# Kernel optimization log

Hardware: AMD Instinct MI355X
Metric: run time of the kernel (lower is better)

The kernel has to match this reference:

```python
import jax, jax.numpy as jnp
import numpy as np

NUM_EMBED = 512
EMBED_DIM = 64
COMMITMENT_COST = 0.25
DECAY = 0.99
LAPLACE_ALPHA = 1e-05


def setup_inputs() -> dict:
    key = jax.random.key(0)
    k1, k2 = jax.random.split(key, 2)
    inputs = jax.random.normal(k1, (4, EMBED_DIM, 32, 32, 32), dtype=jnp.float32)
    embed = jax.random.normal(k2, (NUM_EMBED, EMBED_DIM), dtype=jnp.float32)
    # buffers: embed_avg starts as a clone of embed; cluster_size at steady state (post first pass)
    embed_avg = embed
    cluster_size = jnp.ones((NUM_EMBED,), dtype=jnp.float32)
    return {"inputs": inputs, "embed": embed, "embed_avg": embed_avg, "cluster_size": cluster_size}


def reference(inputs, embed, embed_avg, cluster_size):
    # channel-last flatten: [B,C,D,H,W] -> [B,D,H,W,C] -> [N,C]
    channel_last = jnp.transpose(inputs, (0, 2, 3, 4, 1))
    input_shape = channel_last.shape
    flat_input = channel_last.reshape(-1, EMBED_DIM)  # [N, C]
    n_tokens = flat_input.shape[0]

    distances = ((flat_input ** 2).sum(axis=1, keepdims=True)
                 + (embed ** 2).sum(axis=1)
                 - 2.0 * flat_input @ embed.T)
    encoding_indices = jnp.argmin(distances, axis=1)  # [N]

    quantized_cl = embed[encoding_indices].reshape(input_shape)  # gather + reshape

    # --- EMA codebook update (training branch), all non-differentiable ---
    # new_cluster_size = one_hot.sum(0); dw = one_hot.T @ flat_input  (as segment sums)
    new_counts = jax.ops.segment_sum(jnp.ones((n_tokens,), flat_input.dtype),
                                     encoding_indices, num_segments=NUM_EMBED)
    dw = jax.ops.segment_sum(flat_input, encoding_indices, num_segments=NUM_EMBED)  # [K, C]
    new_cluster_size = cluster_size * DECAY + (1.0 - DECAY) * new_counts
    new_embed_avg = embed_avg * DECAY + (1.0 - DECAY) * dw
    n = new_cluster_size.sum()
    smoothed = n * ((new_cluster_size + LAPLACE_ALPHA) / (n + NUM_EMBED * LAPLACE_ALPHA))
    new_embed = new_embed_avg / smoothed[:, None]

    # perplexity from empirical code usage
    avg_probs = new_counts / n_tokens
    perplexity = jnp.exp(-jnp.sum(avg_probs * jnp.log(avg_probs + 1e-10)))

    quantized_cf = jnp.transpose(quantized_cl, (0, 4, 1, 2, 3))  # back to [B,C,D,H,W]

    # commitment loss (quantized is detached in original; everything above is no_grad)
    e_latent_loss = jnp.mean((quantized_cf - inputs) ** 2)
    loss = COMMITMENT_COST * e_latent_loss

    # straight-through estimator
    quantized_out = inputs + jax.lax.stop_gradient(quantized_cf - inputs)

    encoding_indices = encoding_indices.reshape(input_shape[:-1])
    return (loss, quantized_out, perplexity, encoding_indices,
            new_embed, new_cluster_size, new_embed_avg)
```

## Files before the change

kernel.cpp:

```cpp
#include <hip/hip_runtime.h>
#include <math.h>

typedef __attribute__((ext_vector_type(8))) short s16x8;
typedef __attribute__((ext_vector_type(4))) float f32x4;

#define B_    4
#define C_    64
#define S_    32768
#define N_    131072
#define K_    512
#define SPLITS 8
#define DECAY_ 0.99f
#define ONEM_  0.01f
#define ALPHA_ 1e-5f
#define DELTA_ 0.01f
#define AMB_CAP 65536

#define OFF_LOSS 0
#define OFF_Q    1
#define OFF_PERP 8388609
#define OFF_IDX  8388610
#define OFF_NEMB 8519682
#define OFF_NCS  8552450
#define OFF_NEA  8552962

#define WS_LOSS   0
#define WS_AMBN   8
#define WS_CNT    16
#define WS_CUR    528
#define WS_OFFS   1040
#define WS_SMOOTH 1552
#define WS_E2     2064
#define WS_SORT   2576
#define WS_PART   133648
#define WS_SPL    395792
#define WS_AMB    444944
#define WS_ET     510480

__device__ __forceinline__ ushort f2bf(float f) {
    uint u = __float_as_uint(f);
    u = u + 0x7FFFu + ((u >> 16) & 1u);
    return (ushort)(u >> 16);
}
__device__ __forceinline__ float bf2f(ushort h) {
    return __uint_as_float(((uint)h) << 16);
}

__global__ __launch_bounds__(256) void k_split(const float* __restrict__ embed,
                                               float* __restrict__ wsf,
                                               int* __restrict__ wsi) {
    const int t = threadIdx.x;
    const int lane = t & 63;
    const int code = blockIdx.x * 4 + (t >> 6);
    if (blockIdx.x == 0) {
        for (int i = t; i < WS_OFFS; i += 256) wsi[i] = 0;
    }
    const float e = embed[code * C_ + lane];
    const float sc = -2.f * e;
    const ushort h1 = f2bf(sc);
    const ushort h2 = f2bf(sc - bf2f(h1));
    ushort* tab = (ushort*)(wsf + WS_SPL);
    tab[0 * (K_ * C_) + code * C_ + lane] = h1;
    tab[1 * (K_ * C_) + code * C_ + lane] = h2;
    wsf[WS_ET + lane * K_ + code] = e;
    float sq = e * e;
    for (int o = 32; o > 0; o >>= 1) sq += __shfl_down(sq, o, 64);
    if (lane == 0) wsf[WS_E2 + code] = sq;
}

__global__ __launch_bounds__(256) void k_assign(const float* __restrict__ in,
                                                float* __restrict__ out,
                                                float* __restrict__ wsf,
                                                int* __restrict__ wsi) {
    __shared__ float s_e2l[K_];
    __shared__ int   s_cnt[K_];
    __shared__ float s_x2[256];
    __shared__ float s_loss;

    const int t = threadIdx.x;
    const int lane = t & 63;
    const int w = t >> 6;
    const int col = lane & 15;
    const int quad = lane >> 4;

    for (int i = t; i < K_; i += 256) { s_e2l[i] = wsf[WS_E2 + i]; s_cnt[i] = 0; }
    if (t == 0) s_loss = 0.f;

    const int nw = blockIdx.x * 256 + w * 64;

    s16x8 a[4][2][2];
#pragma unroll
    for (int j = 0; j < 4; ++j) {
        const int n = nw + j * 16 + col;
        const int base = ((n >> 15) << 21) + (n & (S_ - 1));
        float x0[8], x1[8];
#pragma unroll
        for (int q = 0; q < 8; ++q) {
            x0[q] = in[base + ((quad * 8 + q) << 15)];
            x1[q] = in[base + ((32 + quad * 8 + q) << 15)];
        }
        float x2 = 0.f;
#pragma unroll
        for (int q = 0; q < 8; ++q) x2 += x0[q] * x0[q] + x1[q] * x1[q];
        x2 += __shfl_xor(x2, 16, 64);
        x2 += __shfl_xor(x2, 32, 64);
        if (quad == 0) s_x2[w * 64 + j * 16 + col] = x2;

        float4* q0 = (float4*)(out + OFF_Q + (size_t)n * C_ + quad * 8);
        q0[0] = make_float4(x0[0], x0[1], x0[2], x0[3]);
        q0[1] = make_float4(x0[4], x0[5], x0[6], x0[7]);
        float4* q1 = (float4*)(out + OFF_Q + (size_t)n * C_ + 32 + quad * 8);
        q1[0] = make_float4(x1[0], x1[1], x1[2], x1[3]);
        q1[1] = make_float4(x1[4], x1[5], x1[6], x1[7]);

#pragma unroll
        for (int q = 0; q < 8; ++q) {
            ushort h = f2bf(x0[q]); a[j][0][0][q] = (short)h;
            a[j][1][0][q] = (short)f2bf(x0[q] - bf2f(h));
            h = f2bf(x1[q]); a[j][0][1][q] = (short)h;
            a[j][1][1][q] = (short)f2bf(x1[q] - bf2f(h));
        }
    }
    __syncthreads();

    const s16x8* tab = (const s16x8*)(wsf + WS_SPL);
    float bestd[4][4], bestd2[4][4];
    int   besti[4][4];
#pragma unroll
    for (int j = 0; j < 4; ++j)
#pragma unroll
        for (int r = 0; r < 4; ++r) { bestd[j][r] = 3.4e38f; bestd2[j][r] = 3.4e38f; besti[j][r] = 0; }

    int o = col * 8 + quad;
    s16x8 bh0 = tab[o], bh1 = tab[o + 4];
    s16x8 bl0 = tab[4096 + o], bl1 = tab[4096 + o + 4];

    for (int ct = 0; ct < 32; ++ct) {
        s16x8 nh0, nh1, nl0, nl1;
        if (ct < 31) {
            const int on = o + 128;
            nh0 = tab[on];        nh1 = tab[on + 4];
            nl0 = tab[4096 + on]; nl1 = tab[4096 + on + 4];
        }
        const float e2c = s_e2l[ct * 16 + col];
        f32x4 acc[4];
#pragma unroll
        for (int j = 0; j < 4; ++j) acc[j] = (f32x4){e2c, e2c, e2c, e2c};
#pragma unroll
        for (int j = 0; j < 4; ++j) acc[j] = __builtin_amdgcn_mfma_f32_16x16x32_bf16(a[j][1][0], bh0, acc[j], 0, 0, 0);
#pragma unroll
        for (int j = 0; j < 4; ++j) acc[j] = __builtin_amdgcn_mfma_f32_16x16x32_bf16(a[j][1][1], bh1, acc[j], 0, 0, 0);
#pragma unroll
        for (int j = 0; j < 4; ++j) acc[j] = __builtin_amdgcn_mfma_f32_16x16x32_bf16(a[j][0][0], bl0, acc[j], 0, 0, 0);
#pragma unroll
        for (int j = 0; j < 4; ++j) acc[j] = __builtin_amdgcn_mfma_f32_16x16x32_bf16(a[j][0][1], bl1, acc[j], 0, 0, 0);
#pragma unroll
        for (int j = 0; j < 4; ++j) acc[j] = __builtin_amdgcn_mfma_f32_16x16x32_bf16(a[j][0][0], bh0, acc[j], 0, 0, 0);
#pragma unroll
        for (int j = 0; j < 4; ++j) acc[j] = __builtin_amdgcn_mfma_f32_16x16x32_bf16(a[j][0][1], bh1, acc[j], 0, 0, 0);

        const int code = ct * 16 + col;
#pragma unroll
        for (int j = 0; j < 4; ++j) {
#pragma unroll
            for (int r = 0; r < 4; ++r) {
                const float av = acc[j][r];
                bestd2[j][r] = fminf(bestd2[j][r], fmaxf(av, bestd[j][r]));
                if (av < bestd[j][r]) { bestd[j][r] = av; besti[j][r] = code; }
            }
        }
        bh0 = nh0; bh1 = nh1; bl0 = nl0; bl1 = nl1;
        o += 128;
    }

    float lsum = 0.f;
#pragma unroll
    for (int j = 0; j < 4; ++j) {
#pragma unroll
        for (int r = 0; r < 4; ++r) {
            float d1 = bestd[j][r], d2 = bestd2[j][r]; int i1 = besti[j][r];
            for (int m = 1; m <= 8; m <<= 1) {
                const float d1o = __shfl_xor(d1, m, 64);
                const int   i1o = __shfl_xor(i1, m, 64);
                const float d2o = __shfl_xor(d2, m, 64);
                if (d1o < d1 || (d1o == d1 && i1o < i1)) {
                    d2 = fminf(d1, d2o); d1 = d1o; i1 = i1o;
                } else {
                    d2 = fminf(d2, d1o);
                }
            }
            if (col == 0) {
                const int tok = j * 16 + quad * 4 + r;
                out[OFF_IDX + nw + tok] = (float)i1;
                atomicAdd(&s_cnt[i1], 1);
                lsum += d1 + s_x2[w * 64 + tok];
                if (d2 - d1 < DELTA_) {
                    const int pos = atomicAdd(&wsi[WS_AMBN], 1);
                    if (pos < AMB_CAP) wsi[WS_AMB + pos] = nw + tok;
                }
            }
        }
    }
    if (col == 0) atomicAdd(&s_loss, lsum);
    __syncthreads();
    for (int i = t; i < K_; i += 256) {
        const int v = s_cnt[i];
        if (v) atomicAdd(&wsi[WS_CNT + i], v);
    }
    if (t == 0) atomicAdd(&wsf[WS_LOSS], s_loss);
}

__global__ __launch_bounds__(256) void k_fixup(float* __restrict__ out,
                                               const float* __restrict__ wsf,
                                               int* __restrict__ wsi) {
    __shared__ float sx[4][C_];
    const int t = threadIdx.x;
    const int lane = t & 63;
    const int w = t >> 6;
    const int gw = blockIdx.x * 4 + w;
    const int nw = gridDim.x * 4;
    int cntA = wsi[WS_AMBN];
    if (cntA > AMB_CAP) cntA = AMB_CAP;
    const float* eT = wsf + WS_ET;

    for (int a = gw; a < cntA; a += nw) {
        const int n = wsi[WS_AMB + a];
        const float xv = out[OFF_Q + (size_t)n * C_ + lane];
        sx[w][lane] = xv;
        float x2 = xv * xv;
        for (int m = 1; m <= 32; m <<= 1) x2 += __shfl_xor(x2, m, 64);

        float bd = 3.4e38f; int bi = 0;
#pragma unroll 2
        for (int q = 0; q < 8; ++q) {
            const int k = (q << 6) + lane;
            float d0 = 0.f, d1 = 0.f, d2 = 0.f, d3 = 0.f;
#pragma unroll
            for (int c = 0; c < C_; c += 4) {
                d0 += sx[w][c + 0] * eT[(c + 0) * K_ + k];
                d1 += sx[w][c + 1] * eT[(c + 1) * K_ + k];
                d2 += sx[w][c + 2] * eT[(c + 2) * K_ + k];
                d3 += sx[w][c + 3] * eT[(c + 3) * K_ + k];
            }
            const float dist = x2 + wsf[WS_E2 + k] - 2.f * ((d0 + d1) + (d2 + d3));
            if (dist < bd) { bd = dist; bi = k; }
        }
        for (int m = 1; m <= 32; m <<= 1) {
            const float db = __shfl_xor(bd, m, 64);
            const int   ib = __shfl_xor(bi, m, 64);
            if (db < bd || (db == bd && ib < bi)) { bd = db; bi = ib; }
        }
        if (lane == 0) {
            const int old = (int)out[OFF_IDX + n];
            if (bi != old) {
                out[OFF_IDX + n] = (float)bi;
                atomicAdd(&wsi[WS_CNT + old], -1);
                atomicAdd(&wsi[WS_CNT + bi], 1);
            }
        }
    }
}

#define SCT 1024
__global__ __launch_bounds__(256) void k_scatter(const float* __restrict__ out,
                                                 int* __restrict__ wsi) {
    __shared__ int sA[K_];
    __shared__ int sB[K_];
    __shared__ int lc[K_];
    __shared__ int codes[SCT];
    const int t = threadIdx.x;
    const int base = blockIdx.x * SCT;

    const int c0 = wsi[WS_CNT + t];
    const int c1 = wsi[WS_CNT + t + 256];
    sA[t] = c0; sA[t + 256] = c1;
    __syncthreads();
    int* sa = sA; int* sb = sB;
    for (int o = 1; o < K_; o <<= 1) {
        const int va = sa[t]       + ((t >= o)       ? sa[t - o]       : 0);
        const int vb = sa[t + 256] + ((t + 256 >= o) ? sa[t + 256 - o] : 0);
        sb[t] = va; sb[t + 256] = vb;
        __syncthreads();
        int* tmp = sa; sa = sb; sb = tmp;
    }
    const int offs0 = sa[t] - c0;
    const int offs1 = sa[t + 256] - c1;
    if (blockIdx.x == 0) { wsi[WS_OFFS + t] = offs0; wsi[WS_OFFS + t + 256] = offs1; }

    int* hist = sb;
    hist[t] = 0; hist[t + 256] = 0;
    lc[t] = 0;  lc[t + 256] = 0;
    __syncthreads();
#pragma unroll
    for (int j = 0; j < SCT / 256; ++j) {
        const int k = (int)out[OFF_IDX + base + j * 256 + t];
        codes[j * 256 + t] = k;
        atomicAdd(&hist[k], 1);
    }
    __syncthreads();
    const int ha = hist[t];
    const int hb = hist[t + 256];
    int ga = 0, gb = 0;
    if (ha > 0) ga = atomicAdd(&wsi[WS_CUR + t], ha);
    if (hb > 0) gb = atomicAdd(&wsi[WS_CUR + t + 256], hb);
    __syncthreads();
    hist[t] = offs0 + ga;
    hist[t + 256] = offs1 + gb;
    __syncthreads();
#pragma unroll
    for (int j = 0; j < SCT / 256; ++j) {
        const int k = codes[j * 256 + t];
        const int pos = atomicAdd(&lc[k], 1);
        wsi[WS_SORT + hist[k] + pos] = base + j * 256 + t;
    }
}

__global__ __launch_bounds__(64) void k_dw_split(float* __restrict__ out,
                                                 float* __restrict__ wsf,
                                                 const int* __restrict__ wsi) {
    const int lane = threadIdx.x;
    const int k = blockIdx.x >> 3;
    const int p = blockIdx.x & (SPLITS - 1);
    const int off = wsi[WS_OFFS + k];
    const int cnt = wsi[WS_CNT + k];
    const int chunk = (cnt + SPLITS - 1) >> 3;
    const int j0 = p * chunk;
    const int j1 = min(j0 + chunk, cnt);
    const float* fx = out + OFF_Q;
    const int* sort = wsi + WS_SORT + off;

    float acc = 0.f;
    for (int base = j0; base < j1; base += 64) {
        const int mcnt = min(64, j1 - base);
        int id = 0;
        if (base + lane < j1) id = sort[base + lane];
        int m = 0;
        for (; m + 8 <= mcnt; m += 8) {
            const int t0 = __shfl(id, m + 0, 64);
            const int t1 = __shfl(id, m + 1, 64);
            const int t2 = __shfl(id, m + 2, 64);
            const int t3 = __shfl(id, m + 3, 64);
            const int t4 = __shfl(id, m + 4, 64);
            const int t5 = __shfl(id, m + 5, 64);
            const int t6 = __shfl(id, m + 6, 64);
            const int t7 = __shfl(id, m + 7, 64);
            const float v0 = fx[(size_t)t0 * C_ + lane];
            const float v1 = fx[(size_t)t1 * C_ + lane];
            const float v2 = fx[(size_t)t2 * C_ + lane];
            const float v3 = fx[(size_t)t3 * C_ + lane];
            const float v4 = fx[(size_t)t4 * C_ + lane];
            const float v5 = fx[(size_t)t5 * C_ + lane];
            const float v6 = fx[(size_t)t6 * C_ + lane];
            const float v7 = fx[(size_t)t7 * C_ + lane];
            acc += ((v0 + v1) + (v2 + v3)) + ((v4 + v5) + (v6 + v7));
        }
        for (; m < mcnt; ++m) {
            const int tk = __shfl(id, m, 64);
            acc += fx[(size_t)tk * C_ + lane];
        }
    }
    wsf[WS_PART + (size_t)blockIdx.x * C_ + lane] = acc;
}

__global__ __launch_bounds__(256) void k_emaq(const float* __restrict__ embed,
                                              const float* __restrict__ embed_avg,
                                              const float* __restrict__ cs,
                                              float* __restrict__ out,
                                              const float* __restrict__ wsf,
                                              const int* __restrict__ wsi) {
    __shared__ float sn[256];
    __shared__ float sncs[K_];
    const int t = threadIdx.x;
    const int bid = blockIdx.x;

    const int c0 = wsi[WS_CNT + t];
    const int c1 = wsi[WS_CNT + t + 256];
    const float ncs0 = cs[t] * DECAY_ + ONEM_ * (float)c0;
    const float ncs1 = cs[t + 256] * DECAY_ + ONEM_ * (float)c1;
    sncs[t] = ncs0; sncs[t + 256] = ncs1;
    sn[t] = ncs0 + ncs1;
    __syncthreads();
    for (int o = 128; o > 0; o >>= 1) { if (t < o) sn[t] += sn[t + o]; __syncthreads(); }
    const float ntot = sn[0];
    __syncthreads();

    if (bid == 0) {
        out[OFF_NCS + t] = ncs0;
        out[OFF_NCS + t + 256] = ncs1;
        const float ap0 = (float)c0 / (float)N_;
        const float ap1 = (float)c1 / (float)N_;
        sn[t] = ap0 * logf(ap0 + 1e-10f) + ap1 * logf(ap1 + 1e-10f);
        __syncthreads();
        for (int o = 128; o > 0; o >>= 1) { if (t < o) sn[t] += sn[t + o]; __syncthreads(); }
        if (t == 0) {
            out[OFF_PERP] = expf(-sn[0]);
            out[OFF_LOSS] = 0.25f * wsf[WS_LOSS] / (float)((long long)N_ * C_);
        }
    }

    if (bid < 128) {
        const int i = bid * 256 + t;
        const int k = i >> 6;
        const int c = i & 63;
        const float smooth = ntot * (sncs[k] + ALPHA_) / (ntot + (float)K_ * ALPHA_);
        float dw = 0.f;
#pragma unroll
        for (int p = 0; p < SPLITS; ++p)
            dw += wsf[WS_PART + (size_t)(k * SPLITS + p) * C_ + c];
        const float nea = embed_avg[i] * DECAY_ + ONEM_ * dw;
        out[OFF_NEA + i] = nea;
        out[OFF_NEMB + i] = nea / smooth;
    }

    const int n = bid * 256 + t;
    const int b = n >> 15;
    const int s = n & (S_ - 1);
    const int qbase = (b << 21) + s;
    const int k = (int)out[OFF_IDX + n];
    const float4* er = (const float4*)(embed + k * C_);
#pragma unroll
    for (int q = 0; q < 16; ++q) {
        float4 v = er[q];
        out[OFF_Q + qbase + ((4 * q + 0) << 15)] = v.x;
        out[OFF_Q + qbase + ((4 * q + 1) << 15)] = v.y;
        out[OFF_Q + qbase + ((4 * q + 2) << 15)] = v.z;
        out[OFF_Q + qbase + ((4 * q + 3) << 15)] = v.w;
    }
}

extern "C" void kernel_launch(void* const* d_in, const int* in_sizes, int n_in,
                              void* d_out, int out_size, void* d_ws, size_t ws_size,
                              hipStream_t stream) {
    const float* in        = (const float*)d_in[0];
    const float* embed     = (const float*)d_in[1];
    const float* embed_avg = (const float*)d_in[2];
    const float* cs        = (const float*)d_in[3];
    float* out = (float*)d_out;
    float* wsf = (float*)d_ws;
    int*   wsi = (int*)d_ws;

    k_split   <<<K_ / 4, 256, 0, stream>>>(embed, wsf, wsi);
    k_assign  <<<N_ / 256, 256, 0, stream>>>(in, out, wsf, wsi);
    k_fixup   <<<256, 256, 0, stream>>>(out, wsf, wsi);
    k_scatter <<<N_ / SCT, 256, 0, stream>>>(out, wsi);
    k_dw_split<<<K_ * SPLITS, 64, 0, stream>>>(out, wsf, wsi);
    k_emaq    <<<N_ / 256, 256, 0, stream>>>(embed, embed_avg, cs, out, wsf, wsi);
}
```

Baseline: 203.5 us.

## Fuse five post-split kernels into one persistent kernel with grid barriers

Merges the assign, fixup, scatter, dw-split and EMA/quantize kernels into a single 512-block kernel. The stages are separated by software grid-wide barriers built on an atomic counter in workspace. This removes four kernel launches and their inter-kernel gaps. The risks are spin-wait cost at each barrier, fewer blocks for the fixup and dw phases, and deadlock if the 512 blocks cannot all be resident at once.

```diff
diff --git a/kernel.cpp b/kernel.cpp
--- a/kernel.cpp
+++ b/kernel.cpp
@@ -15,6 +15,7 @@
 #define ALPHA_ 1e-5f
 #define DELTA_ 0.01f
 #define AMB_CAP 65536
+#define NB_   512
 
 #define OFF_LOSS 0
 #define OFF_Q    1
@@ -29,7 +30,7 @@
 #define WS_CNT    16
 #define WS_CUR    528
 #define WS_OFFS   1040
-#define WS_SMOOTH 1552
+#define WS_BAR    1552
 #define WS_E2     2064
 #define WS_SORT   2576
 #define WS_PART   133648
@@ -44,6 +45,17 @@
 }
 __device__ __forceinline__ float bf2f(ushort h) {
     return __uint_as_float(((uint)h) << 16);
+}
+
+__device__ __forceinline__ void gbar(int* bar, int target) {
+    __syncthreads();
+    if (threadIdx.x == 0) {
+        __threadfence();
+        atomicAdd(bar, 1);
+        while (atomicAdd(bar, 0) < target) __builtin_amdgcn_s_sleep(8);
+        __threadfence();
+    }
+    __syncthreads();
 }
 
 __global__ __launch_bounds__(256) void k_split(const float* __restrict__ embed,
@@ -54,6 +66,7 @@
     const int code = blockIdx.x * 4 + (t >> 6);
     if (blockIdx.x == 0) {
         for (int i = t; i < WS_OFFS; i += 256) wsi[i] = 0;
+        if (t == 0) wsi[WS_BAR] = 0;
     }
     const float e = embed[code * C_ + lane];
     const float sc = -2.f * e;
@@ -68,363 +81,361 @@
     if (lane == 0) wsf[WS_E2 + code] = sq;
 }
 
-__global__ __launch_bounds__(256) void k_assign(const float* __restrict__ in,
-                                                float* __restrict__ out,
-                                                float* __restrict__ wsf,
-                                                int* __restrict__ wsi) {
-    __shared__ float s_e2l[K_];
-    __shared__ int   s_cnt[K_];
-    __shared__ float s_x2[256];
-    __shared__ float s_loss;
+#define SCT 1024
+__global__ __launch_bounds__(256) void k_fused(const float* __restrict__ in,
+                                               const float* __restrict__ embed,
+                                               const float* __restrict__ embed_avg,
+                                               const float* __restrict__ cs,
+                                               float* __restrict__ out,
+                                               float* wsf,
+                                               int* wsi) {
+    __shared__ int smem[2560];
+    int* bar = wsi + WS_BAR;
 
     const int t = threadIdx.x;
+    const int bid = blockIdx.x;
     const int lane = t & 63;
     const int w = t >> 6;
-    const int col = lane & 15;
-    const int quad = lane >> 4;
-
-    for (int i = t; i < K_; i += 256) { s_e2l[i] = wsf[WS_E2 + i]; s_cnt[i] = 0; }
-    if (t == 0) s_loss = 0.f;
-
-    const int nw = blockIdx.x * 256 + w * 64;
-
-    s16x8 a[4][2][2];
-#pragma unroll
-    for (int j = 0; j < 4; ++j) {
-        const int n = nw + j * 16 + col;
-        const int base = ((n >> 15) << 21) + (n & (S_ - 1));
-        float x0[8], x1[8];
-#pragma unroll
-        for (int q = 0; q < 8; ++q) {
-            x0[q] = in[base + ((quad * 8 + q) << 15)];
-            x1[q] = in[base + ((32 + quad * 8 + q) << 15)];
-        }
-        float x2 = 0.f;
-#pragma unroll
-        for (int q = 0; q < 8; ++q) x2 += x0[q] * x0[q] + x1[q] * x1[q];
-        x2 += __shfl_xor(x2, 16, 64);
-        x2 += __shfl_xor(x2, 32, 64);
-        if (quad == 0) s_x2[w * 64 + j * 16 + col] = x2;
-
-        float4* q0 = (float4*)(out + OFF_Q + (size_t)n * C_ + quad * 8);
-        q0[0] = make_float4(x0[0], x0[1], x0[2], x0[3]);
-        q0[1] = make_float4(x0[4], x0[5], x0[6], x0[7]);
-        float4* q1 = (float4*)(out + OFF_Q + (size_t)n * C_ + 32 + quad * 8);
-        q1[0] = make_float4(x1[0], x1[1], x1[2], x1[3]);
-        q1[1] = make_float4(x1[4], x1[5], x1[6], x1[7]);
-
-#pragma unroll
-        for (int q = 0; q < 8; ++q) {
-            ushort h = f2bf(x0[q]); a[j][0][0][q] = (short)h;
-            a[j][1][0][q] = (short)f2bf(x0[q] - bf2f(h));
-            h = f2bf(x1[q]); a[j][0][1][q] = (short)h;
-            a[j][1][1][q] = (short)f2bf(x1[q] - bf2f(h));
-        }
-    }
-    __syncthreads();
-
-    const s16x8* tab = (const s16x8*)(wsf + WS_SPL);
-    float bestd[4][4], bestd2[4][4];
-    int   besti[4][4];
-#pragma unroll
-    for (int j = 0; j < 4; ++j)
-#pragma unroll
-        for (int r = 0; r < 4; ++r) { bestd[j][r] = 3.4e38f; bestd2[j][r] = 3.4e38f; besti[j][r] = 0; }
-
-    int o = col * 8 + quad;
-    s16x8 bh0 = tab[o], bh1 = tab[o + 4];
-    s16x8 bl0 = tab[4096 + o], bl1 = tab[4096 + o + 4];
-
-    for (int ct = 0; ct < 32; ++ct) {
-        s16x8 nh0, nh1, nl0, nl1;
-        if (ct < 31) {
-            const int on = o + 128;
-            nh0 = tab[on];        nh1 = tab[on + 4];
-            nl0 = tab[4096 + on]; nl1 = tab[4096 + on + 4];
-        }
-        const float e2c = s_e2l[ct * 16 + col];
-        f32x4 acc[4];
-#pragma unroll
-        for (int j = 0; j < 4; ++j) acc[j] = (f32x4){e2c, e2c, e2c, e2c};
-#pragma unroll
-        for (int j = 0; j < 4; ++j) acc[j] = __builtin_amdgcn_mfma_f32_16x16x32_bf16(a[j][1][0], bh0, acc[j], 0, 0, 0);
-#pragma unroll
-        for (int j = 0; j < 4; ++j) acc[j] = __builtin_amdgcn_mfma_f32_16x16x32_bf16(a[j][1][1], bh1, acc[j], 0, 0, 0);
-#pragma unroll
-        for (int j = 0; j < 4; ++j) acc[j] = __builtin_amdgcn_mfma_f32_16x16x32_bf16(a[j][0][0], bl0, acc[j], 0, 0, 0);
-#pragma unroll
-        for (int j = 0; j < 4; ++j) acc[j] = __builtin_amdgcn_mfma_f32_16x16x32_bf16(a[j][0][1], bl1, acc[j], 0, 0, 0);
-#pragma unroll
-        for (int j = 0; j < 4; ++j) acc[j] = __builtin_amdgcn_mfma_f32_16x16x32_bf16(a[j][0][0], bh0, acc[j], 0, 0, 0);
-#pragma unroll
-        for (int j = 0; j < 4; ++j) acc[j] = __builtin_amdgcn_mfma_f32_16x16x32_bf16(a[j][0][1], bh1, acc[j], 0, 0, 0);
-
-        const int code = ct * 16 + col;
+
+    {
+        float* s_e2l  = (float*)smem;
+        int*   s_cnt  = smem + 512;
+        float* s_x2   = (float*)(smem + 1024);
+        float* s_loss = (float*)(smem + 1280);
+
+        const int col = lane & 15;
+        const int quad = lane >> 4;
+
+        for (int i = t; i < K_; i += 256) { s_e2l[i] = wsf[WS_E2 + i]; s_cnt[i] = 0; }
+        if (t == 0) *s_loss = 0.f;
+
+        const int nw = bid * 256 + w * 64;
+
+        s16x8 a[4][2][2];
 #pragma unroll
         for (int j = 0; j < 4; ++j) {
+            const int n = nw + j * 16 + col;
+            const int base = ((n >> 15) << 21) + (n & (S_ - 1));
+            float x0[8], x1[8];
+#pragma unroll
+            for (int q = 0; q < 8; ++q) {
+                x0[q] = in[base + ((quad * 8 + q) << 15)];
+                x1[q] = in[base + ((32 + quad * 8 + q) << 15)];
+            }
+            float x2 = 0.f;
+#pragma unroll
+            for (int q = 0; q < 8; ++q) x2 += x0[q] * x0[q] + x1[q] * x1[q];
+            x2 += __shfl_xor(x2, 16, 64);
+            x2 += __shfl_xor(x2, 32, 64);
+            if (quad == 0) s_x2[w * 64 + j * 16 + col] = x2;
+
+            float4* q0 = (float4*)(out + OFF_Q + (size_t)n * C_ + quad * 8);
+            q0[0] = make_float4(x0[0], x0[1], x0[2], x0[3]);
+            q0[1] = make_float4(x0[4], x0[5], x0[6], x0[7]);
+            float4* q1 = (float4*)(out + OFF_Q + (size_t)n * C_ + 32 + quad * 8);
+            q1[0] = make_float4(x1[0], x1[1], x1[2], x1[3]);
+            q1[1] = make_float4(x1[4], x1[5], x1[6], x1[7]);
+
+#pragma unroll
+            for (int q = 0; q < 8; ++q) {
+                ushort h = f2bf(x0[q]); a[j][0][0][q] = (short)h;
+                a[j][1][0][q] = (short)f2bf(x0[q] - bf2f(h));
+                h = f2bf(x1[q]); a[j][0][1][q] = (short)h;
+                a[j][1][1][q] = (short)f2bf(x1[q] - bf2f(h));
+            }
+        }
+        __syncthreads();
+
+        const s16x8* tab = (const s16x8*)(wsf + WS_SPL);
+        float bestd[4][4], bestd2[4][4];
+        int   besti[4][4];
+#pragma unroll
+        for (int j = 0; j < 4; ++j)
+#pragma unroll
+            for (int r = 0; r < 4; ++r) { bestd[j][r] = 3.4e38f; bestd2[j][r] = 3.4e38f; besti[j][r] = 0; }
+
+        int o = col * 8 + quad;
+        s16x8 bh0 = tab[o], bh1 = tab[o + 4];
+        s16x8 bl0 = tab[4096 + o], bl1 = tab[4096 + o + 4];
+
+        for (int ct = 0; ct < 32; ++ct) {
+            s16x8 nh0, nh1, nl0, nl1;
+            if (ct < 31) {
+                const int on = o + 128;
+                nh0 = tab[on];        nh1 = tab[on + 4];
+                nl0 = tab[4096 + on]; nl1 = tab[4096 + on + 4];
+            }
+            const float e2c = s_e2l[ct * 16 + col];
+            f32x4 acc[4];
+#pragma unroll
+            for (int j = 0; j < 4; ++j) acc[j] = (f32x4){e2c, e2c, e2c, e2c};
+#pragma unroll
+            for (int j = 0; j < 4; ++j) acc[j] = __builtin_amdgcn_mfma_f32_16x16x32_bf16(a[j][1][0], bh0, acc[j], 0, 0, 0);
+#pragma unroll
+            for (int j = 0; j < 4; ++j) acc[j] = __builtin_amdgcn_mfma_f32_16x16x32_bf16(a[j][1][1], bh1, acc[j], 0, 0, 0);
+#pragma unroll
+            for (int j = 0; j < 4; ++j) acc[j] = __builtin_amdgcn_mfma_f32_16x16x32_bf16(a[j][0][0], bl0, acc[j], 0, 0, 0);
+#pragma unroll
+            for (int j = 0; j < 4; ++j) acc[j] = __builtin_amdgcn_mfma_f32_16x16x32_bf16(a[j][0][1], bl1, acc[j], 0, 0, 0);
+#pragma unroll
+            for (int j = 0; j < 4; ++j) acc[j] = __builtin_amdgcn_mfma_f32_16x16x32_bf16(a[j][0][0], bh0, acc[j], 0, 0, 0);
+#pragma unroll
+            for (int j = 0; j < 4; ++j) acc[j] = __builtin_amdgcn_mfma_f32_16x16x32_bf16(a[j][0][1], bh1, acc[j], 0, 0, 0);
+
+            const int code = ct * 16 + col;
+#pragma unroll
+            for (int j = 0; j < 4; ++j) {
+#pragma unroll
+                for (int r = 0; r < 4; ++r) {
+                    const float av = acc[j][r];
+                    bestd2[j][r] = fminf(bestd2[j][r], fmaxf(av, bestd[j][r]));
+                    if (av < bestd[j][r]) { bestd[j][r] = av; besti[j][r] = code; }
+                }
+            }
+            bh0 = nh0; bh1 = nh1; bl0 = nl0; bl1 = nl1;
+            o += 128;
+        }
+
+        float lsum = 0.f;
+#pragma unroll
+        for (int j = 0; j < 4; ++j) {
 #pragma unroll
             for (int r = 0; r < 4; ++r) {
-                const float av = acc[j][r];
-                bestd2[j][r] = fminf(bestd2[j][r], fmaxf(av, bestd[j][r]));
-                if (av < bestd[j][r]) { bestd[j][r] = av; besti[j][r] = code; }
-            }
-        }
-        bh0 = nh0; bh1 = nh1; bl0 = nl0; bl1 = nl1;
-        o += 128;
-    }
-
-    float lsum = 0.f;
-#pragma unroll
-    for (int j = 0; j < 4; ++j) {
-#pragma unroll
-        for (int r = 0; r < 4; ++r) {
-            float d1 = bestd[j][r], d2 = bestd2[j][r]; int i1 = besti[j][r];
-            for (int m = 1; m <= 8; m <<= 1) {
-                const float d1o = __shfl_xor(d1, m, 64);
-                const int   i1o = __shfl_xor(i1, m, 64);
-                const float d2o = __shfl_xor(d2, m, 64);
-                if (d1o < d1 || (d1o == d1 && i1o < i1)) {
-                    d2 = fminf(d1, d2o); d1 = d1o; i1 = i1o;
-                } else {
-                    d2 = fminf(d2, d1o);
-                }
-            }
-            if (col == 0) {
-                const int tok = j * 16 + quad * 4 + r;
-                out[OFF_IDX + nw + tok] = (float)i1;
-                atomicAdd(&s_cnt[i1], 1);
-                lsum += d1 + s_x2[w * 64 + tok];
-                if (d2 - d1 < DELTA_) {
-                    const int pos = atomicAdd(&wsi[WS_AMBN], 1);
-                    if (pos < AMB_CAP) wsi[WS_AMB + pos] = nw + tok;
-                }
-            }
-        }
-    }
-    if (col == 0) atomicAdd(&s_loss, lsum);
-    __syncthreads();
-    for (int i = t; i < K_; i += 256) {
-        const int v = s_cnt[i];
-        if (v) atomicAdd(&wsi[WS_CNT + i], v);
-    }
-    if (t == 0) atomicAdd(&wsf[WS_LOSS], s_loss);
-}
-
-__global__ __launch_bounds__(256) void k_fixup(float* __restrict__ out,
-                                               const float* __restrict__ wsf,
-                                               int* __restrict__ wsi) {
-    __shared__ float sx[4][C_];
-    const int t = threadIdx.x;
-    const int lane = t & 63;
-    const int w = t >> 6;
-    const int gw = blockIdx.x * 4 + w;
-    const int nw = gridDim.x * 4;
-    int cntA = wsi[WS_AMBN];
-    if (cntA > AMB_CAP) cntA = AMB_CAP;
-    const float* eT = wsf + WS_ET;
-
-    for (int a = gw; a < cntA; a += nw) {
-        const int n = wsi[WS_AMB + a];
-        const float xv = out[OFF_Q + (size_t)n * C_ + lane];
-        sx[w][lane] = xv;
-        float x2 = xv * xv;
-        for (int m = 1; m <= 32; m <<= 1) x2 += __shfl_xor(x2, m, 64);
-
-        float bd = 3.4e38f; int bi = 0;
+                float d1 = bestd[j][r], d2 = bestd2[j][r]; int i1 = besti[j][r];
+                for (int m = 1; m <= 8; m <<= 1) {
+                    const float d1o = __shfl_xor(d1, m, 64);
+                    const int   i1o = __shfl_xor(i1, m, 64);
+                    const float d2o = __shfl_xor(d2, m, 64);
+                    if (d1o < d1 || (d1o == d1 && i1o < i1)) {
+                        d2 = fminf(d1, d2o); d1 = d1o; i1 = i1o;
+                    } else {
+                        d2 = fminf(d2, d1o);
+                    }
+                }
+                if (col == 0) {
+                    const int tok = j * 16 + quad * 4 + r;
+                    out[OFF_IDX + nw + tok] = (float)i1;
+                    atomicAdd(&s_cnt[i1], 1);
+                    lsum += d1 + s_x2[w * 64 + tok];
+                    if (d2 - d1 < DELTA_) {
+                        const int pos = atomicAdd(&wsi[WS_AMBN], 1);
+                        if (pos < AMB_CAP) wsi[WS_AMB + pos] = nw + tok;
+                    }
+                }
+            }
+        }
+        if (col == 0) atomicAdd(s_loss, lsum);
+        __syncthreads();
+        for (int i = t; i < K_; i += 256) {
+            const int v = s_cnt[i];
+            if (v) atomicAdd(&wsi[WS_CNT + i], v);
+        }
+        if (t == 0) atomicAdd(&wsf[WS_LOSS], *s_loss);
+    }
+    gbar(bar, NB_ * 1);
+
+    {
+        float (*sx)[C_] = (float (*)[C_])smem;
+        const int gw = bid * 4 + w;
+        int cntA = wsi[WS_AMBN];
+        if (cntA > AMB_CAP) cntA = AMB_CAP;
+        const float* eT = wsf + WS_ET;
+
+        for (int a = gw; a < cntA; a += NB_ * 4) {
+            const int n = wsi[WS_AMB + a];
+            const float xv = out[OFF_Q + (size_t)n * C_ + lane];
+            sx[w][lane] = xv;
+            float x2 = xv * xv;
+            for (int m = 1; m <= 32; m <<= 1) x2 += __shfl_xor(x2, m, 64);
+
+            float bd = 3.4e38f; int bi = 0;
 #pragma unroll 2
-        for (int q = 0; q < 8; ++q) {
-            const int k = (q << 6) + lane;
-            float d0 = 0.f, d1 = 0.f, d2 = 0.f, d3 = 0.f;
-#pragma unroll
-            for (int c = 0; c < C_; c += 4) {
-                d0 += sx[w][c + 0] * eT[(c + 0) * K_ + k];
-                d1 += sx[w][c + 1] * eT[(c + 1) * K_ + k];
-                d2 += sx[w][c + 2] * eT[(c + 2) * K_ + k];
-                d3 += sx[w][c + 3] * eT[(c + 3) * K_ + k];
-            }
-            const float dist = x2 + wsf[WS_E2 + k] - 2.f * ((d0 + d1) + (d2 + d3));
-            if (dist < bd) { bd = dist; bi = k; }
-        }
-        for (int m = 1; m <= 32; m <<= 1) {
-            const float db = __shfl_xor(bd, m, 64);
-            const int   ib = __shfl_xor(bi, m, 64);
-            if (db < bd || (db == bd && ib < bi)) { bd = db; bi = ib; }
-        }
-        if (lane == 0) {
-            const int old = (int)out[OFF_IDX + n];
-            if (bi != old) {
-                out[OFF_IDX + n] = (float)bi;
-                atomicAdd(&wsi[WS_CNT + old], -1);
-                atomicAdd(&wsi[WS_CNT + bi], 1);
-            }
-        }
-    }
-}
-
-#define SCT 1024
-__global__ __launch_bounds__(256) void k_scatter(const float* __restrict__ out,
-                                                 int* __restrict__ wsi) {
-    __shared__ int sA[K_];
-    __shared__ int sB[K_];
-    __shared__ int lc[K_];
-    __shared__ int codes[SCT];
-    const int t = threadIdx.x;
-    const int base = blockIdx.x * SCT;
-
-    const int c0 = wsi[WS_CNT + t];
-    const int c1 = wsi[WS_CNT + t + 256];
-    sA[t] = c0; sA[t + 256] = c1;
-    __syncthreads();
-    int* sa = sA; int* sb = sB;
-    for (int o = 1; o < K_; o <<= 1) {
-        const int va = sa[t]       + ((t >= o)       ? sa[t - o]       : 0);
-        const int vb = sa[t + 256] + ((t + 256 >= o) ? sa[t + 256 - o] : 0);
-        sb[t] = va; sb[t + 256] = vb;
-        __syncthreads();
-        int* tmp = sa; sa = sb; sb = tmp;
-    }
-    const int offs0 = sa[t] - c0;
-    const int offs1 = sa[t + 256] - c1;
-    if (blockIdx.x == 0) { wsi[WS_OFFS + t] = offs0; wsi[WS_OFFS + t + 256] = offs1; }
-
-    int* hist = sb;
-    hist[t] = 0; hist[t + 256] = 0;
-    lc[t] = 0;  lc[t + 256] = 0;
-    __syncthreads();
-#pragma unroll
-    for (int j = 0; j < SCT / 256; ++j) {
-        const int k = (int)out[OFF_IDX + base + j * 256 + t];
-        codes[j * 256 + t] = k;
-        atomicAdd(&hist[k], 1);
-    }
-    __syncthreads();
-    const int ha = hist[t];
-    const int hb = hist[t + 256];
-    int ga = 0, gb = 0;
-    if (ha > 0) ga = atomicAdd(&wsi[WS_CUR + t], ha);
-    if (hb > 0) gb = atomicAdd(&wsi[WS_CUR + t + 256], hb);
-    __syncthreads();
-    hist[t] = offs0 + ga;
-    hist[t + 256] = offs1 + gb;
-    __syncthreads();
-#pragma unroll
-    for (int j = 0; j < SCT / 256; ++j) {
-        const int k = codes[j * 256 + t];
-        const int pos = atomicAdd(&lc[k], 1);
-        wsi[WS_SORT + hist[k] + pos] = base + j * 256 + t;
-    }
-}
-
-__global__ __launch_bounds__(64) void k_dw_split(float* __restrict__ out,
-                                                 float* __restrict__ wsf,
-                                                 const int* __restrict__ wsi) {
-    const int lane = threadIdx.x;
-    const int k = blockIdx.x >> 3;
-    const int p = blockIdx.x & (SPLITS - 1);
-    const int off = wsi[WS_OFFS + k];
-    const int cnt = wsi[WS_CNT + k];
-    const int chunk = (cnt + SPLITS - 1) >> 3;
-    const int j0 = p * chunk;
-    const int j1 = min(j0 + chunk, cnt);
-    const float* fx = out + OFF_Q;
-    const int* sort = wsi + WS_SORT + off;
-
-    float acc = 0.f;
-    for (int base = j0; base < j1; base += 64) {
-        const int mcnt = min(64, j1 - base);
-        int id = 0;
-        if (base + lane < j1) id = sort[base + lane];
-        int m = 0;
-        for (; m + 8 <= mcnt; m += 8) {
-            const int t0 = __shfl(id, m + 0, 64);
-            const int t1 = __shfl(id, m + 1, 64);
-            const int t2 = __shfl(id, m + 2, 64);
-            const int t3 = __shfl(id, m + 3, 64);
-            const int t4 = __shfl(id, m + 4, 64);
-            const int t5 = __shfl(id, m + 5, 64);
-            const int t6 = __shfl(id, m + 6, 64);
-            const int t7 = __shfl(id, m + 7, 64);
-            const float v0 = fx[(size_t)t0 * C_ + lane];
-            const float v1 = fx[(size_t)t1 * C_ + lane];
-            const float v2 = fx[(size_t)t2 * C_ + lane];
-            const float v3 = fx[(size_t)t3 * C_ + lane];
-            const float v4 = fx[(size_t)t4 * C_ + lane];
-            const float v5 = fx[(size_t)t5 * C_ + lane];
-            const float v6 = fx[(size_t)t6 * C_ + lane];
-            const float v7 = fx[(size_t)t7 * C_ + lane];
-            acc += ((v0 + v1) + (v2 + v3)) + ((v4 + v5) + (v6 + v7));
-        }
-        for (; m < mcnt; ++m) {
-            const int tk = __shfl(id, m, 64);
-            acc += fx[(size_t)tk * C_ + lane];
-        }
-    }
-    wsf[WS_PART + (size_t)blockIdx.x * C_ + lane] = acc;
-}
-
-__global__ __launch_bounds__(256) void k_emaq(const float* __restrict__ embed,
-                                              const float* __restrict__ embed_avg,
-                                              const float* __restrict__ cs,
-                                              float* __restrict__ out,
-                                              const float* __restrict__ wsf,
-                                              const int* __restrict__ wsi) {
-    __shared__ float sn[256];
-    __shared__ float sncs[K_];
-    const int t = threadIdx.x;
-    const int bid = blockIdx.x;
-
-    const int c0 = wsi[WS_CNT + t];
-    const int c1 = wsi[WS_CNT + t + 256];
-    const float ncs0 = cs[t] * DECAY_ + ONEM_ * (float)c0;
-    const float ncs1 = cs[t + 256] * DECAY_ + ONEM_ * (float)c1;
-    sncs[t] = ncs0; sncs[t + 256] = ncs1;
-    sn[t] = ncs0 + ncs1;
-    __syncthreads();
-    for (int o = 128; o > 0; o >>= 1) { if (t < o) sn[t] += sn[t + o]; __syncthreads(); }
-    const float ntot = sn[0];
-    __syncthreads();
-
-    if (bid == 0) {
-        out[OFF_NCS + t] = ncs0;
-        out[OFF_NCS + t + 256] = ncs1;
-        const float ap0 = (float)c0 / (float)N_;
-        const float ap1 = (float)c1 / (float)N_;
-        sn[t] = ap0 * logf(ap0 + 1e-10f) + ap1 * logf(ap1 + 1e-10f);
+            for (int q = 0; q < 8; ++q) {
+                const int k = (q << 6) + lane;
+                float d0 = 0.f, d1 = 0.f, d2 = 0.f, d3 = 0.f;
+#pragma unroll
+                for (int c = 0; c < C_; c += 4) {
+                    d0 += sx[w][c + 0] * eT[(c + 0) * K_ + k];
+                    d1 += sx[w][c + 1] * eT[(c + 1) * K_ + k];
+                    d2 += sx[w][c + 2] * eT[(c + 2) * K_ + k];
+                    d3 += sx[w][c + 3] * eT[(c + 3) * K_ + k];
+                }
+                const float dist = x2 + wsf[WS_E2 + k] - 2.f * ((d0 + d1) + (d2 + d3));
+                if (dist < bd) { bd = dist; bi = k; }
+            }
+            for (int m = 1; m <= 32; m <<= 1) {
+                const float db = __shfl_xor(bd, m, 64);
+                const int   ib = __shfl_xor(bi, m, 64);
+                if (db < bd || (db == bd && ib < bi)) { bd = db; bi = ib; }
+            }
+            if (lane == 0) {
+                const int old = (int)out[OFF_IDX + n];
+                if (bi != old) {
+                    out[OFF_IDX + n] = (float)bi;
+                    atomicAdd(&wsi[WS_CNT + old], -1);
+                    atomicAdd(&wsi[WS_CNT + bi], 1);
+                }
+            }
+        }
+    }
+    gbar(bar, NB_ * 2);
+
+    if (bid < 128) {
+        int* sA = smem;
+        int* sB = smem + 512;
+        int* lc = smem + 1024;
+        int* codes = smem + 1536;
+        const int base = bid * SCT;
+
+        const int c0 = wsi[WS_CNT + t];
+        const int c1 = wsi[WS_CNT + t + 256];
+        sA[t] = c0; sA[t + 256] = c1;
+        __syncthreads();
+        int* sa = sA; int* sb = sB;
+        for (int o = 1; o < K_; o <<= 1) {
+            const int va = sa[t]       + ((t >= o)       ? sa[t - o]       : 0);
+            const int vb = sa[t + 256] + ((t + 256 >= o) ? sa[t + 256 - o] : 0);
+            sb[t] = va; sb[t + 256] = vb;
+            __syncthreads();
+            int* tmp = sa; sa = sb; sb = tmp;
+        }
+        const int offs0 = sa[t] - c0;
+        const int offs1 = sa[t + 256] - c1;
+        if (bid == 0) { wsi[WS_OFFS + t] = offs0; wsi[WS_OFFS + t + 256] = offs1; }
+
+        int* hist = sb;
+        hist[t] = 0; hist[t + 256] = 0;
+        lc[t] = 0;  lc[t + 256] = 0;
+        __syncthreads();
+#pragma unroll
+        for (int j = 0; j < SCT / 256; ++j) {
+            const int k = (int)out[OFF_IDX + base + j * 256 + t];
+            codes[j * 256 + t] = k;
+            atomicAdd(&hist[k], 1);
+        }
+        __syncthreads();
+        const int ha = hist[t];
+        const int hb = hist[t + 256];
+        int ga = 0, gb = 0;
+        if (ha > 0) ga = atomicAdd(&wsi[WS_CUR + t], ha);
+        if (hb > 0) gb = atomicAdd(&wsi[WS_CUR + t + 256], hb);
+        __syncthreads();
+        hist[t] = offs0 + ga;
+        hist[t + 256] = offs1 + gb;
+        __syncthreads();
+#pragma unroll
+        for (int j = 0; j < SCT / 256; ++j) {
+            const int k = codes[j * 256 + t];
+            const int pos = atomicAdd(&lc[k], 1);
+            wsi[WS_SORT + hist[k] + pos] = base + j * 256 + t;
+        }
+    }
+    gbar(bar, NB_ * 3);
+
+    {
+        const float* fx = out + OFF_Q;
+        for (int task = bid * 4 + w; task < K_ * SPLITS; task += NB_ * 4) {
+            const int k = task >> 3;
+            const int p = task & (SPLITS - 1);
+            const int off = wsi[WS_OFFS + k];
+            const int cnt = wsi[WS_CNT + k];
+            const int chunk = (cnt + SPLITS - 1) >> 3;
+            const int j0 = p * chunk;
+            const int j1 = min(j0 + chunk, cnt);
+            const int* sort = wsi + WS_SORT + off;
+
+            float acc = 0.f;
+            for (int base = j0; base < j1; base += 64) {
+                const int mcnt = min(64, j1 - base);
+                int id = 0;
+                if (base + lane < j1) id = sort[base + lane];
+                int m = 0;
+                for (; m + 8 <= mcnt; m += 8) {
+                    const int t0 = __shfl(id, m + 0, 64);
+                    const int t1 = __shfl(id, m + 1, 64);
+                    const int t2 = __shfl(id, m + 2, 64);
+                    const int t3 = __shfl(id, m + 3, 64);
+                    const int t4 = __shfl(id, m + 4, 64);
+                    const int t5 = __shfl(id, m + 5, 64);
+                    const int t6 = __shfl(id, m + 6, 64);
+                    const int t7 = __shfl(id, m + 7, 64);
+                    const float v0 = fx[(size_t)t0 * C_ + lane];
+                    const float v1 = fx[(size_t)t1 * C_ + lane];
+                    const float v2 = fx[(size_t)t2 * C_ + lane];
+                    const float v3 = fx[(size_t)t3 * C_ + lane];
+                    const float v4 = fx[(size_t)t4 * C_ + lane];
+                    const float v5 = fx[(size_t)t5 * C_ + lane];
+                    const float v6 = fx[(size_t)t6 * C_ + lane];
+                    const float v7 = fx[(size_t)t7 * C_ + lane];
+                    acc += ((v0 + v1) + (v2 + v3)) + ((v4 + v5) + (v6 + v7));
+                }
+                for (; m < mcnt; ++m) {
+                    const int tk = __shfl(id, m, 64);
+                    acc += fx[(size_t)tk * C_ + lane];
+                }
+            }
+            wsf[WS_PART + (size_t)task * C_ + lane] = acc;
+        }
+    }
+    gbar(bar, NB_ * 4);
+
+    {
+        float* sn   = (float*)smem;
+        float* sncs = (float*)(smem + 256);
+
+        const int c0 = wsi[WS_CNT + t];
+        const int c1 = wsi[WS_CNT + t + 256];
+        const float ncs0 = cs[t] * DECAY_ + ONEM_ * (float)c0;
+        const float ncs1 = cs[t + 256] * DECAY_ + ONEM_ * (float)c1;
+        sncs[t] = ncs0; sncs[t + 256] = ncs1;
+        sn[t] = ncs0 + ncs1;
         __syncthreads();
         for (int o = 128; o > 0; o >>= 1) { if (t < o) sn[t] += sn[t + o]; __syncthreads(); }
-        if (t == 0) {
-            out[OFF_PERP] = expf(-sn[0]);
-            out[OFF_LOSS] = 0.25f * wsf[WS_LOSS] / (float)((long long)N_ * C_);
-        }
-    }
-
-    if (bid < 128) {
-        const int i = bid * 256 + t;
-        const int k = i >> 6;
-        const int c = i & 63;
-        const float smooth = ntot * (sncs[k] + ALPHA_) / (ntot + (float)K_ * ALPHA_);
-        float dw = 0.f;
-#pragma unroll
-        for (int p = 0; p < SPLITS; ++p)
-            dw += wsf[WS_PART + (size_t)(k * SPLITS + p) * C_ + c];
-        const float nea = embed_avg[i] * DECAY_ + ONEM_ * dw;
-        out[OFF_NEA + i] = nea;
-        out[OFF_NEMB + i] = nea / smooth;
-    }
-
-    const int n = bid * 256 + t;
-    const int b = n >> 15;
-    const int s = n & (S_ - 1);
-    const int qbase = (b << 21) + s;
-    const int k = (int)out[OFF_IDX + n];
-    const float4* er = (const float4*)(embed + k * C_);
-#pragma unroll
-    for (int q = 0; q < 16; ++q) {
-        float4 v = er[q];
-        out[OFF_Q + qbase + ((4 * q + 0) << 15)] = v.x;
-        out[OFF_Q + qbase + ((4 * q + 1) << 15)] = v.y;
-        out[OFF_Q + qbase + ((4 * q + 2) << 15)] = v.z;
-        out[OFF_Q + qbase + ((4 * q + 3) << 15)] = v.w;
+        const float ntot = sn[0];
+        __syncthreads();
+
+        if (bid == 0) {
+            out[OFF_NCS + t] = ncs0;
+            out[OFF_NCS + t + 256] = ncs1;
+            const float ap0 = (float)c0 / (float)N_;
+            const float ap1 = (float)c1 / (float)N_;
+            sn[t] = ap0 * logf(ap0 + 1e-10f) + ap1 * logf(ap1 + 1e-10f);
+            __syncthreads();
+            for (int o = 128; o > 0; o >>= 1) { if (t < o) sn[t] += sn[t + o]; __syncthreads(); }
+            if (t == 0) {
+                out[OFF_PERP] = expf(-sn[0]);
+                out[OFF_LOSS] = 0.25f * wsf[WS_LOSS] / (float)((long long)N_ * C_);
+            }
+        }
+
+        if (bid < 128) {
+            const int i = bid * 256 + t;
+            const int k = i >> 6;
+            const int c = i & 63;
+            const float smooth = ntot * (sncs[k] + ALPHA_) / (ntot + (float)K_ * ALPHA_);
+            float dw = 0.f;
+#pragma unroll
+            for (int p = 0; p < SPLITS; ++p)
+                dw += wsf[WS_PART + (size_t)(k * SPLITS + p) * C_ + c];
+            const float nea = embed_avg[i] * DECAY_ + ONEM_ * dw;
+            out[OFF_NEA + i] = nea;
+            out[OFF_NEMB + i] = nea / smooth;
+        }
+
+        const int n = bid * 256 + t;
+        const int b = n >> 15;
+        const int s = n & (S_ - 1);
+        const int qbase = (b << 21) + s;
+        const int k = (int)out[OFF_IDX + n];
+        const float4* er = (const float4*)(embed + k * C_);
+#pragma unroll
+        for (int q = 0; q < 16; ++q) {
+            float4 v = er[q];
+            out[OFF_Q + qbase + ((4 * q + 0) << 15)] = v.x;
+            out[OFF_Q + qbase + ((4 * q + 1) << 15)] = v.y;
+            out[OFF_Q + qbase + ((4 * q + 2) << 15)] = v.z;
+            out[OFF_Q + qbase + ((4 * q + 3) << 15)] = v.w;
+        }
     }
 }
 
@@ -439,10 +450,6 @@
     float* wsf = (float*)d_ws;
     int*   wsi = (int*)d_ws;
 
-    k_split   <<<K_ / 4, 256, 0, stream>>>(embed, wsf, wsi);
-    k_assign  <<<N_ / 256, 256, 0, stream>>>(in, out, wsf, wsi);
-    k_fixup   <<<256, 256, 0, stream>>>(out, wsf, wsi);
-    k_scatter <<<N_ / SCT, 256, 0, stream>>>(out, wsi);
-    k_dw_split<<<K_ * SPLITS, 64, 0, stream>>>(out, wsf, wsi);
-    k_emaq    <<<N_ / 256, 256, 0, stream>>>(embed, embed_avg, cs, out, wsf, wsi);
-}
+    k_split <<<K_ / 4, 256, 0, stream>>>(embed, wsf, wsi);
+    k_fused <<<NB_, 256, 0, stream>>>(in, embed, embed_avg, cs, out, wsf, wsi);
+}
```

Measured after the change: 359.1 us. +76.5%, slower.

## Stage split codebook table in LDS with MFMA-fragment layout

Applied to the files above, without the earlier changes.

The split bf16 codebook table is rearranged in k_split so each code tile's MFMA B-fragments sit next to each other. k_assign now copies it into shared memory in four 32KB chunks and reads fragments from LDS, instead of each wave loading them straight from global or L2. The goal is to cut repeated global traffic and scattered loads on the codebook. In exchange it adds 32KB of LDS per block, which may lower occupancy, plus extra block-wide barriers per chunk.

```diff
diff --git a/kernel.cpp b/kernel.cpp
--- a/kernel.cpp
+++ b/kernel.cpp
@@ -29,7 +29,6 @@
 #define WS_CNT    16
 #define WS_CUR    528
 #define WS_OFFS   1040
-#define WS_SMOOTH 1552
 #define WS_E2     2064
 #define WS_SORT   2576
 #define WS_PART   133648
@@ -59,9 +58,12 @@
     const float sc = -2.f * e;
     const ushort h1 = f2bf(sc);
     const ushort h2 = f2bf(sc - bf2f(h1));
-    ushort* tab = (ushort*)(wsf + WS_SPL);
-    tab[0 * (K_ * C_) + code * C_ + lane] = h1;
-    tab[1 * (K_ * C_) + code * C_ + lane] = h2;
+    ushort* tab2 = (ushort*)(wsf + WS_SPL);
+    const int ct = code >> 4, col = code & 15;
+    const int kt = lane >> 5, q = (lane >> 3) & 3, el = lane & 7;
+    const int base2 = ct * 2048 + kt * 512 + (q * 16 + col) * 8 + el;
+    tab2[base2] = h1;
+    tab2[base2 + 1024] = h2;
     wsf[WS_ET + lane * K_ + code] = e;
     float sq = e * e;
     for (int o = 32; o > 0; o >>= 1) sq += __shfl_down(sq, o, 64);
@@ -72,6 +74,7 @@
                                                 float* __restrict__ out,
                                                 float* __restrict__ wsf,
                                                 int* __restrict__ wsi) {
+    __shared__ ushort s_tab[16384];
     __shared__ float s_e2l[K_];
     __shared__ int   s_cnt[K_];
     __shared__ float s_x2[256];
@@ -121,9 +124,8 @@
             a[j][1][1][q] = (short)f2bf(x1[q] - bf2f(h));
         }
     }
-    __syncthreads();
-
-    const s16x8* tab = (const s16x8*)(wsf + WS_SPL);
+
+    const ushort* gtab = (const ushort*)(wsf + WS_SPL);
     float bestd[4][4], bestd2[4][4];
     int   besti[4][4];
 #pragma unroll
@@ -131,46 +133,58 @@
 #pragma unroll
         for (int r = 0; r < 4; ++r) { bestd[j][r] = 3.4e38f; bestd2[j][r] = 3.4e38f; besti[j][r] = 0; }
 
-    int o = col * 8 + quad;
-    s16x8 bh0 = tab[o], bh1 = tab[o + 4];
-    s16x8 bl0 = tab[4096 + o], bl1 = tab[4096 + o + 4];
-
-    for (int ct = 0; ct < 32; ++ct) {
-        s16x8 nh0, nh1, nl0, nl1;
-        if (ct < 31) {
-            const int on = o + 128;
-            nh0 = tab[on];        nh1 = tab[on + 4];
-            nl0 = tab[4096 + on]; nl1 = tab[4096 + on + 4];
-        }
-        const float e2c = s_e2l[ct * 16 + col];
-        f32x4 acc[4];
-#pragma unroll
-        for (int j = 0; j < 4; ++j) acc[j] = (f32x4){e2c, e2c, e2c, e2c};
-#pragma unroll
-        for (int j = 0; j < 4; ++j) acc[j] = __builtin_amdgcn_mfma_f32_16x16x32_bf16(a[j][1][0], bh0, acc[j], 0, 0, 0);
-#pragma unroll
-        for (int j = 0; j < 4; ++j) acc[j] = __builtin_amdgcn_mfma_f32_16x16x32_bf16(a[j][1][1], bh1, acc[j], 0, 0, 0);
-#pragma unroll
-        for (int j = 0; j < 4; ++j) acc[j] = __builtin_amdgcn_mfma_f32_16x16x32_bf16(a[j][0][0], bl0, acc[j], 0, 0, 0);
-#pragma unroll
-        for (int j = 0; j < 4; ++j) acc[j] = __builtin_amdgcn_mfma_f32_16x16x32_bf16(a[j][0][1], bl1, acc[j], 0, 0, 0);
-#pragma unroll
-        for (int j = 0; j < 4; ++j) acc[j] = __builtin_amdgcn_mfma_f32_16x16x32_bf16(a[j][0][0], bh0, acc[j], 0, 0, 0);
-#pragma unroll
-        for (int j = 0; j < 4; ++j) acc[j] = __builtin_amdgcn_mfma_f32_16x16x32_bf16(a[j][0][1], bh1, acc[j], 0, 0, 0);
-
-        const int code = ct * 16 + col;
-#pragma unroll
-        for (int j = 0; j < 4; ++j) {
-#pragma unroll
-            for (int r = 0; r < 4; ++r) {
-                const float av = acc[j][r];
-                bestd2[j][r] = fminf(bestd2[j][r], fmaxf(av, bestd[j][r]));
-                if (av < bestd[j][r]) { bestd[j][r] = av; besti[j][r] = code; }
-            }
-        }
-        bh0 = nh0; bh1 = nh1; bl0 = nl0; bl1 = nl1;
-        o += 128;
+    for (int qh = 0; qh < 4; ++qh) {
+        __syncthreads();
+#pragma unroll
+        for (int it = 0; it < 8; ++it) {
+            const int idx = (it * 256 + t) * 8;
+            *(uint4*)&s_tab[idx] = *(const uint4*)&gtab[qh * 16384 + idx];
+        }
+        __syncthreads();
+
+        const s16x8* ltab = (const s16x8*)s_tab;
+        int lo = lane;
+        s16x8 bh0 = ltab[lo],       bh1 = ltab[lo + 64];
+        s16x8 bl0 = ltab[lo + 128], bl1 = ltab[lo + 192];
+
+        for (int cc = 0; cc < 8; ++cc) {
+            const int ct = qh * 8 + cc;
+            s16x8 nh0, nh1, nl0, nl1;
+            if (cc < 7) {
+                const int on = lo + 256;
+                nh0 = ltab[on];       nh1 = ltab[on + 64];
+                nl0 = ltab[on + 128]; nl1 = ltab[on + 192];
+            }
+            const float e2c = s_e2l[ct * 16 + col];
+            f32x4 acc[4];
+#pragma unroll
+            for (int j = 0; j < 4; ++j) acc[j] = (f32x4){e2c, e2c, e2c, e2c};
+#pragma unroll
+            for (int j = 0; j < 4; ++j) acc[j] = __builtin_amdgcn_mfma_f32_16x16x32_bf16(a[j][1][0], bh0, acc[j], 0, 0, 0);
+#pragma unroll
+            for (int j = 0; j < 4; ++j) acc[j] = __builtin_amdgcn_mfma_f32_16x16x32_bf16(a[j][1][1], bh1, acc[j], 0, 0, 0);
+#pragma unroll
+            for (int j = 0; j < 4; ++j) acc[j] = __builtin_amdgcn_mfma_f32_16x16x32_bf16(a[j][0][0], bl0, acc[j], 0, 0, 0);
+#pragma unroll
+            for (int j = 0; j < 4; ++j) acc[j] = __builtin_amdgcn_mfma_f32_16x16x32_bf16(a[j][0][1], bl1, acc[j], 0, 0, 0);
+#pragma unroll
+            for (int j = 0; j < 4; ++j) acc[j] = __builtin_amdgcn_mfma_f32_16x16x32_bf16(a[j][0][0], bh0, acc[j], 0, 0, 0);
+#pragma unroll
+            for (int j = 0; j < 4; ++j) acc[j] = __builtin_amdgcn_mfma_f32_16x16x32_bf16(a[j][0][1], bh1, acc[j], 0, 0, 0);
+
+            const int code = ct * 16 + col;
+#pragma unroll
+            for (int j = 0; j < 4; ++j) {
+#pragma unroll
+                for (int r = 0; r < 4; ++r) {
+                    const float av = acc[j][r];
+                    bestd2[j][r] = fminf(bestd2[j][r], fmaxf(av, bestd[j][r]));
+                    if (av < bestd[j][r]) { bestd[j][r] = av; besti[j][r] = code; }
+                }
+            }
+            bh0 = nh0; bh1 = nh1; bl0 = nl0; bl1 = nl1;
+            lo += 256;
+        }
     }
 
     float lsum = 0.f;
```

Measured after the change: 197.8 us, median of 2. 2.8% less time.
